# Optimization experiments

Hardware: AMD Instinct MI355X
Metric: run time of the kernel (lower is better)

Reference implementation:

```python
import jax, jax.numpy as jnp
import numpy as np
from jax import lax


def _conv1d(z, w):
    # z: [B, C_in, L], w: [C_out, C_in, K], stride 1, padding 1 -> [B, C_out, L]
    return lax.conv_general_dilated(
        z, w, window_strides=(1,), padding=[(1, 1)],
        dimension_numbers=("NCH", "OIH", "NCH"))


def setup_inputs() -> dict:
    key = jax.random.key(0)
    k1, k2, k3 = jax.random.split(key, 3)
    B, T, C, H, L, K = 16, 64, 128, 256, 128, 3
    x = jax.random.normal(k1, (B, T, C, L), dtype=jnp.float32)
    # small init so tanh stays in its useful range
    W_i = jax.random.normal(k2, (H, C, K), dtype=jnp.float32) * 0.05
    W_h = jax.random.normal(k3, (H, H, K), dtype=jnp.float32) * 0.05
    return {"x": x, "W_i": W_i, "W_h": W_h}


def reference(x, W_i, W_h):
    # Conv1DRnn, single layer, unidirectional, no bias, mode RNN_TANH:
    #   h_t = tanh(conv_i(x_t) + conv_h(h_{t-1}))
    # x: [B, T, C, L] -> out: [B, T, H, L]
    B, T, C, L = x.shape
    H = W_i.shape[0]
    h0 = jnp.zeros((B, H, L), dtype=x.dtype)
    xt = jnp.swapaxes(x, 0, 1)  # [T, B, C, L]

    def step(h, x_t):
        h_new = jnp.tanh(_conv1d(x_t, W_i) + _conv1d(h, W_h))
        return h_new, h_new

    _, hs = lax.scan(step, h0, xt)  # hs: [T, B, H, L]
    return jnp.swapaxes(hs, 0, 1)   # [B, T, H, L]
```

## Files before the change

kernel.cpp:

```cpp
#include <hip/hip_runtime.h>
#include <math.h>

typedef _Float16 f16;
typedef _Float16 f16x2 __attribute__((ext_vector_type(2)));
typedef _Float16 f16x8 __attribute__((ext_vector_type(8)));
typedef float f32x4 __attribute__((ext_vector_type(4)));
typedef unsigned long long u64;

#define LDIM 128
#define HOUT 256

#define XB0 18432

__device__ __forceinline__ float tanh_fast(float x) {
    float a = fabsf(x);
    float e = __expf(-2.0f * a);
    float r = (1.0f - e) / (1.0f + e);
    return copysignf(r, x);
}

__device__ __forceinline__ void st_mb(u64* p, u64 v) {
    __hip_atomic_store(p, v, __ATOMIC_RELAXED, __HIP_MEMORY_SCOPE_AGENT);
}
__device__ __forceinline__ u64 ld_mb(const u64* p) {
    return __hip_atomic_load(p, __ATOMIC_RELAXED, __HIP_MEMORY_SCOPE_AGENT);
}

__global__ void prep_w(const float* __restrict__ wi, f16* __restrict__ wtif,
                       const float* __restrict__ wh, f16* __restrict__ wthf)
{
    int idx = blockIdx.x * 256 + threadIdx.x;
    const int ni = 3 * 4 * 16 * 64 * 8;
    if (idx < ni) {
        int j    = idx & 7;
        int lane = (idx >> 3) & 63;
        int h16  = (idx >> 9) & 15;
        int kk   = (idx >> 13) & 3;
        int s    = idx >> 15;
        int h = h16 * 16 + (lane & 15);
        int c = kk * 32 + (lane >> 4) * 8 + j;
        wtif[idx] = (f16)wi[(h * 128 + c) * 3 + s];
    } else {
        int e = idx - ni;
        if (e >= 3 * 8 * 16 * 64 * 8) return;
        int j    = e & 7;
        int lane = (e >> 3) & 63;
        int h16  = (e >> 9) & 15;
        int kk   = (e >> 13) & 7;
        int s    = e >> 16;
        int h = h16 * 16 + (lane & 15);
        int c = kk * 32 + (lane >> 4) * 8 + j;
        wthf[e] = (f16)wh[(h * 256 + c) * 3 + s];
    }
}

__device__ __forceinline__ void stage_x(char* xp, const float* __restrict__ xt,
                                        int l0, int tid)
{
    const int c = tid >> 2, q = tid & 3;
    f32x4 v = *(const f32x4*)(xt + c * LDIM + l0 + q * 4);
#pragma unroll
    for (int i = 0; i < 4; ++i) {
        int r = q * 4 + i + 1;
        float xx = v[i];
        f16 h = (f16)xx, lo = (f16)(xx - (float)h);
        int off = r * 256 + ((((c >> 3) ^ (r & 7)) << 4)) + (c & 7) * 2;
        *(f16*)(xp + off) = h;
        *(f16*)(xp + 4608 + off) = lo;
    }
    if (tid < 256) {
        int e = tid >> 7, cc = tid & 127;
        int l = e ? l0 + 16 : l0 - 1;
        int r = e ? 17 : 0;
        float xx = ((unsigned)l < 128u) ? xt[cc * LDIM + l] : 0.f;
        f16 h = (f16)xx, lo = (f16)(xx - (float)h);
        int off = r * 256 + ((((cc >> 3) ^ (r & 7)) << 4)) + (cc & 7) * 2;
        *(f16*)(xp + off) = h;
        *(f16*)(xp + 4608 + off) = lo;
    }
}

__device__ __forceinline__ void zconv(const char* xp, const f16* __restrict__ wti,
                                      int wid, int lane, int l16, int g, f32x4 zn[2])
{
#pragma unroll
    for (int kk = 0; kk < 4; ++kk) {
#pragma unroll
        for (int s = 0; s < 3; ++s) {
            f16x8 a0 = *(const f16x8*)(wti +
                ((((s * 4 + kk) * 16 + wid * 2 + 0) * 64 + lane) << 3));
            f16x8 a1 = *(const f16x8*)(wti +
                ((((s * 4 + kk) * 16 + wid * 2 + 1) * 64 + lane) << 3));
            int r = l16 + s;
            int base = r * 256 + ((((kk * 4 + g) ^ (r & 7)) << 4));
            f16x8 b0 = *(const f16x8*)(xp + base);
            f16x8 b1 = *(const f16x8*)(xp + 4608 + base);
            zn[0] = __builtin_amdgcn_mfma_f32_16x16x32_f16(a0, b0, zn[0], 0, 0, 0);
            zn[0] = __builtin_amdgcn_mfma_f32_16x16x32_f16(a0, b1, zn[0], 0, 0, 0);
            zn[1] = __builtin_amdgcn_mfma_f32_16x16x32_f16(a1, b0, zn[1], 0, 0, 0);
            zn[1] = __builtin_amdgcn_mfma_f32_16x16x32_f16(a1, b1, zn[1], 0, 0, 0);
        }
    }
}

__device__ __forceinline__ void hconv_s(const char* hp, const f16* __restrict__ wth,
                                        int s, int wid, int lane, int l16, int g,
                                        f32x4 hacc[2])
{
#pragma unroll
    for (int kk = 0; kk < 8; ++kk) {
        f16x8 a0 = *(const f16x8*)(wth +
            ((((s * 8 + kk) * 16 + wid * 2 + 0) * 64 + lane) << 3));
        f16x8 a1 = *(const f16x8*)(wth +
            ((((s * 8 + kk) * 16 + wid * 2 + 1) * 64 + lane) << 3));
        int r = l16 + s;
        int base = r * 512 + ((((kk * 4 + g) ^ (r & 7)) << 4));
        f16x8 b0 = *(const f16x8*)(hp + base);
        hacc[0] = __builtin_amdgcn_mfma_f32_16x16x32_f16(a0, b0, hacc[0], 0, 0, 0);
        hacc[1] = __builtin_amdgcn_mfma_f32_16x16x32_f16(a1, b0, hacc[1], 0, 0, 0);
    }
}

__global__ void __launch_bounds__(512)
rnn_fused(const float* __restrict__ x, const f16* __restrict__ wti,
          const f16* __restrict__ wth, float* __restrict__ out,
          u64* __restrict__ mbox)
{
    __shared__ __align__(16) char smem[36864];
    const int tid  = threadIdx.x;
    const int lane = tid & 63, wid = tid >> 6;
    const int b    = blockIdx.x & 15;
    const int lw   = blockIdx.x >> 4;
    const int l0   = lw * 16;
    const int l16  = lane & 15, g = lane >> 4;
    const long HL  = (long)HOUT * LDIM;
    float* outb    = out + (long)b * (64 * HL);
    const float* xb = x + (long)b * (64L * 128 * LDIM);

    int edge = -1;
    if (l16 == 0  && lw > 0) edge = 0;
    if (l16 == 15 && lw < 7) edge = 1;
    u64* mb_pub = (edge >= 0) ? (mbox + (((b * 8 + lw) * 2 + edge) * 2) * 256) : nullptr;

    stage_x(smem + XB0, xb, l0, tid);
    stage_x(smem + XB0 + 9216, xb + 128 * LDIM, l0, tid);
    __syncthreads();
    f32x4 zcur[2] = {};
    zconv(smem + XB0, wti, wid, lane, l16, g, zcur);
    __syncthreads();

    for (int t = 0; t < 64; ++t) {
        float* outt = outb + (long)t * HL;

        if (t + 2 < 64)
            stage_x(smem + XB0 + (t & 1) * 9216, xb + (long)(t + 2) * (128 * LDIM), l0, tid);

        f32x4 zn[2] = {};
        if (t < 63)
            zconv(smem + XB0 + ((t + 1) & 1) * 9216, wti, wid, lane, l16, g, zn);

        f32x4 hacc[2] = {};
        char* hp = smem + ((t ^ 1) & 1) * 9216;
        if (t > 0)
            hconv_s(hp, wth, 1, wid, lane, l16, g, hacc);

        if (t > 0) {
            const int par = (t ^ 1) & 1;
            if (tid < 256) {
                int c = tid;
                float xx = 0.f;
                if (lw > 0) {
                    const u64* p = mbox + ((((b * 8 + lw - 1) * 2 + 1) * 2 + par) * 256) + c;
                    u64 v = ld_mb(p);
                    while ((unsigned)(v >> 32) < (unsigned)t) {
                        __builtin_amdgcn_s_sleep(1);
                        v = ld_mb(p);
                    }
                    xx = __uint_as_float((unsigned)v);
                }
                int off = ((c >> 3) << 4) + (c & 7) * 2;
                *(f16*)(hp + off) = (f16)xx;
            } else {
                int c = tid - 256;
                float xx = 0.f;
                if (lw < 7) {
                    const u64* p = mbox + ((((b * 8 + lw + 1) * 2 + 0) * 2 + par) * 256) + c;
                    u64 v = ld_mb(p);
                    while ((unsigned)(v >> 32) < (unsigned)t) {
                        __builtin_amdgcn_s_sleep(1);
                        v = ld_mb(p);
                    }
                    xx = __uint_as_float((unsigned)v);
                }
                int off = 17 * 512 + ((((c >> 3) ^ 1) << 4)) + (c & 7) * 2;
                *(f16*)(hp + off) = (f16)xx;
            }
        }
        __syncthreads();

        if (t > 0) {
            hconv_s(hp, wth, 0, wid, lane, l16, g, hacc);
            hconv_s(hp, wth, 2, wid, lane, l16, g, hacc);
        }

        char* pw = smem + (t & 1) * 9216;
        u64* pub = (edge >= 0) ? (mb_pub + (t & 1) * 256) : nullptr;
        const u64 tagw = ((u64)(unsigned)(t + 1)) << 32;
        const int r  = l16 + 1;
        const int rx = r & 7;
        float hv[2][4];
#pragma unroll
        for (int hf = 0; hf < 2; ++hf)
#pragma unroll
            for (int vv = 0; vv < 4; ++vv)
                hv[hf][vv] = tanh_fast(hacc[hf][vv] + zcur[hf][vv]);

        if (edge >= 0) {
#pragma unroll
            for (int hf = 0; hf < 2; ++hf)
#pragma unroll
                for (int vv = 0; vv < 4; ++vv) {
                    int c = wid * 32 + hf * 16 + g * 4 + vv;
                    st_mb(&pub[c], tagw | (u64)__float_as_uint(hv[hf][vv]));
                }
        }
#pragma unroll
        for (int hf = 0; hf < 2; ++hf)
#pragma unroll
            for (int vv = 0; vv < 4; ++vv) {
                int c = wid * 32 + hf * 16 + g * 4 + vv;
                outt[(long)c * LDIM + l0 + l16] = hv[hf][vv];
            }
#pragma unroll
        for (int hf = 0; hf < 2; ++hf)
#pragma unroll
            for (int p = 0; p < 2; ++p) {
                int c = wid * 32 + hf * 16 + g * 4 + p * 2;
                int off = r * 512 + ((((c >> 3) ^ rx) << 4)) + (c & 7) * 2;
                f16x2 hw; hw[0] = (f16)hv[hf][2 * p]; hw[1] = (f16)hv[hf][2 * p + 1];
                *(f16x2*)(pw + off) = hw;
            }
        zcur[0] = zn[0];
        zcur[1] = zn[1];

        __syncthreads();
    }
}

extern "C" void kernel_launch(void* const* d_in, const int* in_sizes, int n_in,
                              void* d_out, int out_size, void* d_ws, size_t ws_size,
                              hipStream_t stream)
{
    const float* x   = (const float*)d_in[0];
    const float* W_i = (const float*)d_in[1];
    const float* W_h = (const float*)d_in[2];
    float* out = (float*)d_out;

    f16* wt_i = (f16*)d_ws;
    f16* wt_h = (f16*)((char*)d_ws + 196608);
    u64* mbox = (u64*)((char*)d_ws + 589824);

    prep_w<<<1152, 256, 0, stream>>>(W_i, wt_i, W_h, wt_h);
    hipMemsetAsync(mbox, 0, 131072, stream);

    rnn_fused<<<128, 512, 0, stream>>>(x, wt_i, wt_h, out, mbox);
}
```

Baseline: 418.7 us.

## Use halo-widened tiles with redundant compute to exchange boundaries every 8 steps

Each block now computes a 32-column window (its 16 owned columns plus an 8-column halo on each side) so that boundary hidden states only need to be exchanged with neighbouring blocks once every 8 timesteps rather than every step. Neighbours publish 9-column packed fp16 halos through a larger mailbox, and blocks only spin-wait at those exchange points. The input-conv prefetch also drops from two steps ahead to one. The aim is to cut the per-step cross-block spin-wait latency at the cost of doubling the MFMA work per step and using more LDS and mailbox memory.

```diff
diff --git a/kernel.cpp b/kernel.cpp
--- a/kernel.cpp
+++ b/kernel.cpp
@@ -10,7 +10,7 @@
 #define LDIM 128
 #define HOUT 256
 
-#define XB0 18432
+#define XP 17408
 
 __device__ __forceinline__ float tanh_fast(float x) {
     float a = fabsf(x);
@@ -24,6 +24,10 @@
 }
 __device__ __forceinline__ u64 ld_mb(const u64* p) {
     return __hip_atomic_load(p, __ATOMIC_RELAXED, __HIP_MEMORY_SCOPE_AGENT);
+}
+__device__ __forceinline__ unsigned pack_h2(float a, float b) {
+    f16x2 t; t[0] = (f16)a; t[1] = (f16)b;
+    unsigned u; __builtin_memcpy(&u, &t, 4); return u;
 }
 
 __global__ void prep_w(const float* __restrict__ wi, f16* __restrict__ wtif,
@@ -58,66 +62,30 @@
                                         int l0, int tid)
 {
     const int c = tid >> 2, q = tid & 3;
-    f32x4 v = *(const f32x4*)(xt + c * LDIM + l0 + q * 4);
-#pragma unroll
-    for (int i = 0; i < 4; ++i) {
-        int r = q * 4 + i + 1;
-        float xx = v[i];
+    const int colStart = l0 - 8 + q * 8;
+    f32x4 v0 = {}, v1 = {};
+    if (colStart >= 0 && colStart + 7 < 128) {
+        v0 = *(const f32x4*)(xt + c * LDIM + colStart);
+        v1 = *(const f32x4*)(xt + c * LDIM + colStart + 4);
+    }
+#pragma unroll
+    for (int i = 0; i < 8; ++i) {
+        int row = q * 8 + i + 1;
+        float xx = (i < 4) ? v0[i] : v1[i - 4];
         f16 h = (f16)xx, lo = (f16)(xx - (float)h);
-        int off = r * 256 + ((((c >> 3) ^ (r & 7)) << 4)) + (c & 7) * 2;
+        int off = row * 256 + ((((c >> 3) ^ (row & 7)) << 4)) + (c & 7) * 2;
         *(f16*)(xp + off) = h;
-        *(f16*)(xp + 4608 + off) = lo;
+        *(f16*)(xp + 8704 + off) = lo;
     }
     if (tid < 256) {
-        int e = tid >> 7, cc = tid & 127;
-        int l = e ? l0 + 16 : l0 - 1;
-        int r = e ? 17 : 0;
-        float xx = ((unsigned)l < 128u) ? xt[cc * LDIM + l] : 0.f;
+        int row = (tid >= 128) ? 33 : 0;
+        int cc  = tid & 127;
+        int col = (row == 0) ? l0 - 9 : l0 + 24;
+        float xx = ((unsigned)col < 128u) ? xt[cc * LDIM + col] : 0.f;
         f16 h = (f16)xx, lo = (f16)(xx - (float)h);
-        int off = r * 256 + ((((cc >> 3) ^ (r & 7)) << 4)) + (cc & 7) * 2;
+        int off = row * 256 + ((((cc >> 3) ^ (row & 7)) << 4)) + (cc & 7) * 2;
         *(f16*)(xp + off) = h;
-        *(f16*)(xp + 4608 + off) = lo;
-    }
-}
-
-__device__ __forceinline__ void zconv(const char* xp, const f16* __restrict__ wti,
-                                      int wid, int lane, int l16, int g, f32x4 zn[2])
-{
-#pragma unroll
-    for (int kk = 0; kk < 4; ++kk) {
-#pragma unroll
-        for (int s = 0; s < 3; ++s) {
-            f16x8 a0 = *(const f16x8*)(wti +
-                ((((s * 4 + kk) * 16 + wid * 2 + 0) * 64 + lane) << 3));
-            f16x8 a1 = *(const f16x8*)(wti +
-                ((((s * 4 + kk) * 16 + wid * 2 + 1) * 64 + lane) << 3));
-            int r = l16 + s;
-            int base = r * 256 + ((((kk * 4 + g) ^ (r & 7)) << 4));
-            f16x8 b0 = *(const f16x8*)(xp + base);
-            f16x8 b1 = *(const f16x8*)(xp + 4608 + base);
-            zn[0] = __builtin_amdgcn_mfma_f32_16x16x32_f16(a0, b0, zn[0], 0, 0, 0);
-            zn[0] = __builtin_amdgcn_mfma_f32_16x16x32_f16(a0, b1, zn[0], 0, 0, 0);
-            zn[1] = __builtin_amdgcn_mfma_f32_16x16x32_f16(a1, b0, zn[1], 0, 0, 0);
-            zn[1] = __builtin_amdgcn_mfma_f32_16x16x32_f16(a1, b1, zn[1], 0, 0, 0);
-        }
-    }
-}
-
-__device__ __forceinline__ void hconv_s(const char* hp, const f16* __restrict__ wth,
-                                        int s, int wid, int lane, int l16, int g,
-                                        f32x4 hacc[2])
-{
-#pragma unroll
-    for (int kk = 0; kk < 8; ++kk) {
-        f16x8 a0 = *(const f16x8*)(wth +
-            ((((s * 8 + kk) * 16 + wid * 2 + 0) * 64 + lane) << 3));
-        f16x8 a1 = *(const f16x8*)(wth +
-            ((((s * 8 + kk) * 16 + wid * 2 + 1) * 64 + lane) << 3));
-        int r = l16 + s;
-        int base = r * 512 + ((((kk * 4 + g) ^ (r & 7)) << 4));
-        f16x8 b0 = *(const f16x8*)(hp + base);
-        hacc[0] = __builtin_amdgcn_mfma_f32_16x16x32_f16(a0, b0, hacc[0], 0, 0, 0);
-        hacc[1] = __builtin_amdgcn_mfma_f32_16x16x32_f16(a1, b0, hacc[1], 0, 0, 0);
+        *(f16*)(xp + 8704 + off) = lo;
     }
 }
 
@@ -126,7 +94,7 @@
           const f16* __restrict__ wth, float* __restrict__ out,
           u64* __restrict__ mbox)
 {
-    __shared__ __align__(16) char smem[36864];
+    __shared__ __align__(16) char smem[52224];
     const int tid  = threadIdx.x;
     const int lane = tid & 63, wid = tid >> 6;
     const int b    = blockIdx.x & 15;
@@ -137,113 +105,168 @@
     float* outb    = out + (long)b * (64 * HL);
     const float* xb = x + (long)b * (64L * 128 * LDIM);
 
-    int edge = -1;
-    if (l16 == 0  && lw > 0) edge = 0;
-    if (l16 == 15 && lw < 7) edge = 1;
-    u64* mb_pub = (edge >= 0) ? (mbox + (((b * 8 + lw) * 2 + edge) * 2) * 256) : nullptr;
-
-    stage_x(smem + XB0, xb, l0, tid);
-    stage_x(smem + XB0 + 9216, xb + 128 * LDIM, l0, tid);
-    __syncthreads();
-    f32x4 zcur[2] = {};
-    zconv(smem + XB0, wti, wid, lane, l16, g, zcur);
+    {
+        int row = (tid >= 256) ? 33 : 0;
+        int cc  = tid & 255;
+        int off = row * 512 + ((((cc >> 3) ^ (row & 7)) << 4)) + (cc & 7) * 2;
+        *(f16*)(smem + off) = (f16)0.f;
+    }
+    stage_x(smem + XP, xb, l0, tid);
     __syncthreads();
 
     for (int t = 0; t < 64; ++t) {
         float* outt = outb + (long)t * HL;
 
-        if (t + 2 < 64)
-            stage_x(smem + XB0 + (t & 1) * 9216, xb + (long)(t + 2) * (128 * LDIM), l0, tid);
-
-        f32x4 zn[2] = {};
-        if (t < 63)
-            zconv(smem + XB0 + ((t + 1) & 1) * 9216, wti, wid, lane, l16, g, zn);
-
-        f32x4 hacc[2] = {};
-        char* hp = smem + ((t ^ 1) & 1) * 9216;
-        if (t > 0)
-            hconv_s(hp, wth, 1, wid, lane, l16, g, hacc);
-
+        if (t + 1 < 64)
+            stage_x(smem + XP + ((t + 1) & 1) * 17408,
+                    xb + (long)(t + 1) * (128 * LDIM), l0, tid);
+
+        f32x4 zcur[2][2] = {};
+        {
+            const char* xp = smem + XP + (t & 1) * 17408;
+#pragma unroll
+            for (int kk = 0; kk < 4; ++kk)
+#pragma unroll
+                for (int s = 0; s < 3; ++s) {
+                    f16x8 a0 = *(const f16x8*)(wti +
+                        ((((s * 4 + kk) * 16 + wid * 2 + 0) * 64 + lane) << 3));
+                    f16x8 a1 = *(const f16x8*)(wti +
+                        ((((s * 4 + kk) * 16 + wid * 2 + 1) * 64 + lane) << 3));
+#pragma unroll
+                    for (int tau = 0; tau < 2; ++tau) {
+                        int r = 16 * tau + l16 + s;
+                        int base = r * 256 + ((((kk * 4 + g) ^ (r & 7)) << 4));
+                        f16x8 bh = *(const f16x8*)(xp + base);
+                        f16x8 bl = *(const f16x8*)(xp + 8704 + base);
+                        zcur[tau][0] = __builtin_amdgcn_mfma_f32_16x16x32_f16(a0, bh, zcur[tau][0], 0, 0, 0);
+                        zcur[tau][0] = __builtin_amdgcn_mfma_f32_16x16x32_f16(a0, bl, zcur[tau][0], 0, 0, 0);
+                        zcur[tau][1] = __builtin_amdgcn_mfma_f32_16x16x32_f16(a1, bh, zcur[tau][1], 0, 0, 0);
+                        zcur[tau][1] = __builtin_amdgcn_mfma_f32_16x16x32_f16(a1, bl, zcur[tau][1], 0, 0, 0);
+                    }
+                }
+        }
+
+        f32x4 hacc[2][2] = {};
         if (t > 0) {
-            const int par = (t ^ 1) & 1;
-            if (tid < 256) {
-                int c = tid;
-                float xx = 0.f;
-                if (lw > 0) {
-                    const u64* p = mbox + ((((b * 8 + lw - 1) * 2 + 1) * 2 + par) * 256) + c;
+#pragma unroll
+            for (int kk = 0; kk < 8; ++kk)
+#pragma unroll
+                for (int s = 0; s < 3; ++s) {
+                    f16x8 a0 = *(const f16x8*)(wth +
+                        ((((s * 8 + kk) * 16 + wid * 2 + 0) * 64 + lane) << 3));
+                    f16x8 a1 = *(const f16x8*)(wth +
+                        ((((s * 8 + kk) * 16 + wid * 2 + 1) * 64 + lane) << 3));
+#pragma unroll
+                    for (int tau = 0; tau < 2; ++tau) {
+                        int r = 16 * tau + l16 + s;
+                        int base = r * 512 + ((((kk * 4 + g) ^ (r & 7)) << 4));
+                        f16x8 bb = *(const f16x8*)(smem + base);
+                        hacc[tau][0] = __builtin_amdgcn_mfma_f32_16x16x32_f16(a0, bb, hacc[tau][0], 0, 0, 0);
+                        hacc[tau][1] = __builtin_amdgcn_mfma_f32_16x16x32_f16(a1, bb, hacc[tau][1], 0, 0, 0);
+                    }
+                }
+        }
+        __syncthreads();
+
+        float hv[2][2][4];
+#pragma unroll
+        for (int tau = 0; tau < 2; ++tau)
+#pragma unroll
+            for (int hf = 0; hf < 2; ++hf)
+#pragma unroll
+                for (int vv = 0; vv < 4; ++vv)
+                    hv[tau][hf][vv] = tanh_fast(hacc[tau][hf][vv] + zcur[tau][hf][vv]);
+
+        {
+            const int tsel = (l16 < 8) ? 1 : 0;
+            const int gcs  = l0 + (l16 ^ 8);
+#pragma unroll
+            for (int hf = 0; hf < 2; ++hf)
+#pragma unroll
+                for (int vv = 0; vv < 4; ++vv) {
+                    int c = wid * 32 + hf * 16 + g * 4 + vv;
+                    outt[(long)c * LDIM + gcs] = hv[tsel][hf][vv];
+                }
+        }
+#pragma unroll
+        for (int tau = 0; tau < 2; ++tau) {
+            const int rw = 1 + 16 * tau + l16;
+            const int gc = l0 - 9 + rw;
+            const bool ok = ((unsigned)gc < 128u);
+            const int rx = rw & 7;
+#pragma unroll
+            for (int hf = 0; hf < 2; ++hf)
+#pragma unroll
+                for (int p = 0; p < 2; ++p) {
+                    int c = wid * 32 + hf * 16 + g * 4 + p * 2;
+                    f16x2 w;
+                    w[0] = ok ? (f16)hv[tau][hf][2 * p]     : (f16)0.f;
+                    w[1] = ok ? (f16)hv[tau][hf][2 * p + 1] : (f16)0.f;
+                    int off = rw * 512 + ((((c >> 3) ^ rx) << 4)) + (c & 7) * 2;
+                    *(f16x2*)(smem + off) = w;
+                }
+        }
+        __syncthreads();
+
+        if (t > 0 && (t & 7) == 0 && t <= 56) {
+            const unsigned e = (unsigned)(t >> 3);
+            const int par = e & 1;
+            const u64 tagw = ((u64)e) << 32;
+
+            {
+                int cs = -1, tl = 0;
+                if (l16 >= 8)      { cs = l16 - 8; tl = 0; }
+                else if (l16 == 0) { cs = 8;       tl = 1; }
+                if (cs >= 0 && lw > 0) {
+                    u64* mp = mbox + (((long)(b * 8 + lw) * 2 + 0) * 2 + par) * 1152 + cs * 128;
+#pragma unroll
+                    for (int hf = 0; hf < 2; ++hf)
+#pragma unroll
+                        for (int p = 0; p < 2; ++p) {
+                            int hp = wid * 16 + hf * 8 + g * 2 + p;
+                            st_mb(mp + hp, tagw |
+                                  (u64)pack_h2(hv[tl][hf][2 * p], hv[tl][hf][2 * p + 1]));
+                        }
+                }
+            }
+            {
+                int cs = -1, tr_ = 0;
+                if (l16 == 15)     { cs = 0;        tr_ = 0; }
+                else if (l16 <= 7) { cs = l16 + 1;  tr_ = 1; }
+                if (cs >= 0 && lw < 7) {
+                    u64* mp = mbox + (((long)(b * 8 + lw) * 2 + 1) * 2 + par) * 1152 + cs * 128;
+#pragma unroll
+                    for (int hf = 0; hf < 2; ++hf)
+#pragma unroll
+                        for (int p = 0; p < 2; ++p) {
+                            int hp = wid * 16 + hf * 8 + g * 2 + p;
+                            st_mb(mp + hp, tagw |
+                                  (u64)pack_h2(hv[tr_][hf][2 * p], hv[tr_][hf][2 * p + 1]));
+                        }
+                }
+            }
+            for (int i = tid; i < 2304; i += 512) {
+                int side = (i >= 1152);
+                int j = i - side * 1152;
+                int col = j >> 7, hp = j & 127;
+                int nb = lw + (side ? 1 : -1);
+                if ((unsigned)nb < 8u) {
+                    const u64* p = mbox + (((long)(b * 8 + nb) * 2 + (side ? 0 : 1)) * 2 + par) * 1152 + j;
                     u64 v = ld_mb(p);
-                    while ((unsigned)(v >> 32) < (unsigned)t) {
+                    while ((unsigned)(v >> 32) < e) {
                         __builtin_amdgcn_s_sleep(1);
                         v = ld_mb(p);
                     }
-                    xx = __uint_as_float((unsigned)v);
-                }
-                int off = ((c >> 3) << 4) + (c & 7) * 2;
-                *(f16*)(hp + off) = (f16)xx;
-            } else {
-                int c = tid - 256;
-                float xx = 0.f;
-                if (lw < 7) {
-                    const u64* p = mbox + ((((b * 8 + lw + 1) * 2 + 0) * 2 + par) * 256) + c;
-                    u64 v = ld_mb(p);
-                    while ((unsigned)(v >> 32) < (unsigned)t) {
-                        __builtin_amdgcn_s_sleep(1);
-                        v = ld_mb(p);
-                    }
-                    xx = __uint_as_float((unsigned)v);
-                }
-                int off = 17 * 512 + ((((c >> 3) ^ 1) << 4)) + (c & 7) * 2;
-                *(f16*)(hp + off) = (f16)xx;
+                    unsigned pk = (unsigned)v;
+                    int row = side ? 25 + col : col;
+                    int c = hp * 2;
+                    int off = row * 512 + ((((c >> 3) ^ (row & 7)) << 4)) + (c & 7) * 2;
+                    f16x2 w; __builtin_memcpy(&w, &pk, 4);
+                    *(f16x2*)(smem + off) = w;
+                }
             }
-        }
-        __syncthreads();
-
-        if (t > 0) {
-            hconv_s(hp, wth, 0, wid, lane, l16, g, hacc);
-            hconv_s(hp, wth, 2, wid, lane, l16, g, hacc);
-        }
-
-        char* pw = smem + (t & 1) * 9216;
-        u64* pub = (edge >= 0) ? (mb_pub + (t & 1) * 256) : nullptr;
-        const u64 tagw = ((u64)(unsigned)(t + 1)) << 32;
-        const int r  = l16 + 1;
-        const int rx = r & 7;
-        float hv[2][4];
-#pragma unroll
-        for (int hf = 0; hf < 2; ++hf)
-#pragma unroll
-            for (int vv = 0; vv < 4; ++vv)
-                hv[hf][vv] = tanh_fast(hacc[hf][vv] + zcur[hf][vv]);
-
-        if (edge >= 0) {
-#pragma unroll
-            for (int hf = 0; hf < 2; ++hf)
-#pragma unroll
-                for (int vv = 0; vv < 4; ++vv) {
-                    int c = wid * 32 + hf * 16 + g * 4 + vv;
-                    st_mb(&pub[c], tagw | (u64)__float_as_uint(hv[hf][vv]));
-                }
-        }
-#pragma unroll
-        for (int hf = 0; hf < 2; ++hf)
-#pragma unroll
-            for (int vv = 0; vv < 4; ++vv) {
-                int c = wid * 32 + hf * 16 + g * 4 + vv;
-                outt[(long)c * LDIM + l0 + l16] = hv[hf][vv];
-            }
-#pragma unroll
-        for (int hf = 0; hf < 2; ++hf)
-#pragma unroll
-            for (int p = 0; p < 2; ++p) {
-                int c = wid * 32 + hf * 16 + g * 4 + p * 2;
-                int off = r * 512 + ((((c >> 3) ^ rx) << 4)) + (c & 7) * 2;
-                f16x2 hw; hw[0] = (f16)hv[hf][2 * p]; hw[1] = (f16)hv[hf][2 * p + 1];
-                *(f16x2*)(pw + off) = hw;
-            }
-        zcur[0] = zn[0];
-        zcur[1] = zn[1];
-
-        __syncthreads();
+            __syncthreads();
+        }
     }
 }
 
@@ -261,7 +284,7 @@
     u64* mbox = (u64*)((char*)d_ws + 589824);
 
     prep_w<<<1152, 256, 0, stream>>>(W_i, wt_i, W_h, wt_h);
-    hipMemsetAsync(mbox, 0, 131072, stream);
+    hipMemsetAsync(mbox, 0, 4718592, stream);
 
     rnn_fused<<<128, 512, 0, stream>>>(x, wt_i, wt_h, out, mbox);
 }
```

Result: slower. 572.9 us (+36.8%).

## Keep recurrent weights in registers with 4 waves and drop x split-precision

Applied to the files above, without the earlier changes.

Cuts the block to 256 threads (4 waves, each covering 64 output channels) and preloads all W_h MFMA fragments into registers once, so the per-step recurrent conv no longer reloads weights from global memory. The x-input conv is computed inline each step into the same accumulator instead of being pipelined a step ahead. The hi/lo fp16 split of x is dropped, which halves the MFMA work for the input conv but lowers input precision. The register footprint is very large (96 f16x8 fragments per lane), which risks spills, and there are half as many waves to hide latency.

```diff
diff --git a/kernel.cpp b/kernel.cpp
--- a/kernel.cpp
+++ b/kernel.cpp
@@ -10,7 +10,7 @@
 #define LDIM 128
 #define HOUT 256
 
-#define XB0 18432
+#define XB 18432
 
 __device__ __forceinline__ float tanh_fast(float x) {
     float a = fabsf(x);
@@ -57,76 +57,23 @@
 __device__ __forceinline__ void stage_x(char* xp, const float* __restrict__ xt,
                                         int l0, int tid)
 {
-    const int c = tid >> 2, q = tid & 3;
-    f32x4 v = *(const f32x4*)(xt + c * LDIM + l0 + q * 4);
-#pragma unroll
-    for (int i = 0; i < 4; ++i) {
-        int r = q * 4 + i + 1;
-        float xx = v[i];
-        f16 h = (f16)xx, lo = (f16)(xx - (float)h);
-        int off = r * 256 + ((((c >> 3) ^ (r & 7)) << 4)) + (c & 7) * 2;
-        *(f16*)(xp + off) = h;
-        *(f16*)(xp + 4608 + off) = lo;
+    const int c = tid & 127, half = tid >> 7;
+#pragma unroll
+    for (int i = 0; i < 9; ++i) {
+        int row = half * 9 + i;
+        int col = l0 - 1 + row;
+        float xx = ((unsigned)col < 128u) ? xt[c * LDIM + col] : 0.f;
+        int off = row * 256 + ((((c >> 3) ^ (row & 7)) << 4)) + (c & 7) * 2;
+        *(f16*)(xp + off) = (f16)xx;
     }
-    if (tid < 256) {
-        int e = tid >> 7, cc = tid & 127;
-        int l = e ? l0 + 16 : l0 - 1;
-        int r = e ? 17 : 0;
-        float xx = ((unsigned)l < 128u) ? xt[cc * LDIM + l] : 0.f;
-        f16 h = (f16)xx, lo = (f16)(xx - (float)h);
-        int off = r * 256 + ((((cc >> 3) ^ (r & 7)) << 4)) + (cc & 7) * 2;
-        *(f16*)(xp + off) = h;
-        *(f16*)(xp + 4608 + off) = lo;
-    }
-}
-
-__device__ __forceinline__ void zconv(const char* xp, const f16* __restrict__ wti,
-                                      int wid, int lane, int l16, int g, f32x4 zn[2])
-{
-#pragma unroll
-    for (int kk = 0; kk < 4; ++kk) {
-#pragma unroll
-        for (int s = 0; s < 3; ++s) {
-            f16x8 a0 = *(const f16x8*)(wti +
-                ((((s * 4 + kk) * 16 + wid * 2 + 0) * 64 + lane) << 3));
-            f16x8 a1 = *(const f16x8*)(wti +
-                ((((s * 4 + kk) * 16 + wid * 2 + 1) * 64 + lane) << 3));
-            int r = l16 + s;
-            int base = r * 256 + ((((kk * 4 + g) ^ (r & 7)) << 4));
-            f16x8 b0 = *(const f16x8*)(xp + base);
-            f16x8 b1 = *(const f16x8*)(xp + 4608 + base);
-            zn[0] = __builtin_amdgcn_mfma_f32_16x16x32_f16(a0, b0, zn[0], 0, 0, 0);
-            zn[0] = __builtin_amdgcn_mfma_f32_16x16x32_f16(a0, b1, zn[0], 0, 0, 0);
-            zn[1] = __builtin_amdgcn_mfma_f32_16x16x32_f16(a1, b0, zn[1], 0, 0, 0);
-            zn[1] = __builtin_amdgcn_mfma_f32_16x16x32_f16(a1, b1, zn[1], 0, 0, 0);
-        }
-    }
-}
-
-__device__ __forceinline__ void hconv_s(const char* hp, const f16* __restrict__ wth,
-                                        int s, int wid, int lane, int l16, int g,
-                                        f32x4 hacc[2])
-{
-#pragma unroll
-    for (int kk = 0; kk < 8; ++kk) {
-        f16x8 a0 = *(const f16x8*)(wth +
-            ((((s * 8 + kk) * 16 + wid * 2 + 0) * 64 + lane) << 3));
-        f16x8 a1 = *(const f16x8*)(wth +
-            ((((s * 8 + kk) * 16 + wid * 2 + 1) * 64 + lane) << 3));
-        int r = l16 + s;
-        int base = r * 512 + ((((kk * 4 + g) ^ (r & 7)) << 4));
-        f16x8 b0 = *(const f16x8*)(hp + base);
-        hacc[0] = __builtin_amdgcn_mfma_f32_16x16x32_f16(a0, b0, hacc[0], 0, 0, 0);
-        hacc[1] = __builtin_amdgcn_mfma_f32_16x16x32_f16(a1, b0, hacc[1], 0, 0, 0);
-    }
-}
-
-__global__ void __launch_bounds__(512)
+}
+
+__global__ void __launch_bounds__(256, 1)
 rnn_fused(const float* __restrict__ x, const f16* __restrict__ wti,
           const f16* __restrict__ wth, float* __restrict__ out,
           u64* __restrict__ mbox)
 {
-    __shared__ __align__(16) char smem[36864];
+    __shared__ __align__(16) char smem[27648];
     const int tid  = threadIdx.x;
     const int lane = tid & 63, wid = tid >> 6;
     const int b    = blockIdx.x & 15;
@@ -142,35 +89,76 @@
     if (l16 == 15 && lw < 7) edge = 1;
     u64* mb_pub = (edge >= 0) ? (mbox + (((b * 8 + lw) * 2 + edge) * 2) * 256) : nullptr;
 
-    stage_x(smem + XB0, xb, l0, tid);
-    stage_x(smem + XB0 + 9216, xb + 128 * LDIM, l0, tid);
-    __syncthreads();
-    f32x4 zcur[2] = {};
-    zconv(smem + XB0, wti, wid, lane, l16, g, zcur);
+    f16x8 afrh[3][8][4];
+#pragma unroll
+    for (int s = 0; s < 3; ++s)
+#pragma unroll
+        for (int kk = 0; kk < 8; ++kk)
+#pragma unroll
+            for (int hf = 0; hf < 4; ++hf)
+                afrh[s][kk][hf] = *(const f16x8*)(wth +
+                    ((((s * 8 + kk) * 16 + wid * 4 + hf) * 64 + lane) << 3));
+
+    stage_x(smem + XB, xb, l0, tid);
     __syncthreads();
 
     for (int t = 0; t < 64; ++t) {
         float* outt = outb + (long)t * HL;
 
-        if (t + 2 < 64)
-            stage_x(smem + XB0 + (t & 1) * 9216, xb + (long)(t + 2) * (128 * LDIM), l0, tid);
-
-        f32x4 zn[2] = {};
-        if (t < 63)
-            zconv(smem + XB0 + ((t + 1) & 1) * 9216, wti, wid, lane, l16, g, zn);
-
-        f32x4 hacc[2] = {};
+        if (t + 1 < 64)
+            stage_x(smem + XB + ((t + 1) & 1) * 4608,
+                    xb + (long)(t + 1) * (128 * LDIM), l0, tid);
+
+        f32x4 acc[4] = {};
+        {
+            const char* xp = smem + XB + (t & 1) * 4608;
+#pragma unroll
+            for (int kk = 0; kk < 4; ++kk)
+#pragma unroll
+                for (int s = 0; s < 3; ++s) {
+                    f16x8 a0 = *(const f16x8*)(wti +
+                        ((((s * 4 + kk) * 16 + wid * 4 + 0) * 64 + lane) << 3));
+                    f16x8 a1 = *(const f16x8*)(wti +
+                        ((((s * 4 + kk) * 16 + wid * 4 + 1) * 64 + lane) << 3));
+                    f16x8 a2 = *(const f16x8*)(wti +
+                        ((((s * 4 + kk) * 16 + wid * 4 + 2) * 64 + lane) << 3));
+                    f16x8 a3 = *(const f16x8*)(wti +
+                        ((((s * 4 + kk) * 16 + wid * 4 + 3) * 64 + lane) << 3));
+                    int r = l16 + s;
+                    int base = r * 256 + ((((kk * 4 + g) ^ (r & 7)) << 4));
+                    f16x8 bb = *(const f16x8*)(xp + base);
+                    acc[0] = __builtin_amdgcn_mfma_f32_16x16x32_f16(a0, bb, acc[0], 0, 0, 0);
+                    acc[1] = __builtin_amdgcn_mfma_f32_16x16x32_f16(a1, bb, acc[1], 0, 0, 0);
+                    acc[2] = __builtin_amdgcn_mfma_f32_16x16x32_f16(a2, bb, acc[2], 0, 0, 0);
+                    acc[3] = __builtin_amdgcn_mfma_f32_16x16x32_f16(a3, bb, acc[3], 0, 0, 0);
+                }
+        }
+
         char* hp = smem + ((t ^ 1) & 1) * 9216;
-        if (t > 0)
-            hconv_s(hp, wth, 1, wid, lane, l16, g, hacc);
+
+        if (t > 0) {
+#pragma unroll
+            for (int kk = 0; kk < 8; ++kk) {
+                int r = l16 + 1;
+                int base = r * 512 + ((((kk * 4 + g) ^ (r & 7)) << 4));
+                f16x8 bb = *(const f16x8*)(hp + base);
+#pragma unroll
+                for (int hf = 0; hf < 4; ++hf)
+                    acc[hf] = __builtin_amdgcn_mfma_f32_16x16x32_f16(
+                        afrh[1][kk][hf], bb, acc[hf], 0, 0, 0);
+            }
+        }
 
         if (t > 0) {
             const int par = (t ^ 1) & 1;
-            if (tid < 256) {
+#pragma unroll
+            for (int side = 0; side < 2; ++side) {
                 int c = tid;
+                int nb = lw + (side ? 1 : -1);
                 float xx = 0.f;
-                if (lw > 0) {
-                    const u64* p = mbox + ((((b * 8 + lw - 1) * 2 + 1) * 2 + par) * 256) + c;
+                if ((unsigned)nb < 8u) {
+                    const u64* p = mbox +
+                        ((((b * 8 + nb) * 2 + (side ? 0 : 1)) * 2 + par) * 256) + c;
                     u64 v = ld_mb(p);
                     while ((unsigned)(v >> 32) < (unsigned)t) {
                         __builtin_amdgcn_s_sleep(1);
@@ -178,70 +166,66 @@
                     }
                     xx = __uint_as_float((unsigned)v);
                 }
-                int off = ((c >> 3) << 4) + (c & 7) * 2;
+                int row = side ? 17 : 0;
+                int off = row * 512 + ((((c >> 3) ^ (row & 7)) << 4)) + (c & 7) * 2;
                 *(f16*)(hp + off) = (f16)xx;
-            } else {
-                int c = tid - 256;
-                float xx = 0.f;
-                if (lw < 7) {
-                    const u64* p = mbox + ((((b * 8 + lw + 1) * 2 + 0) * 2 + par) * 256) + c;
-                    u64 v = ld_mb(p);
-                    while ((unsigned)(v >> 32) < (unsigned)t) {
-                        __builtin_amdgcn_s_sleep(1);
-                        v = ld_mb(p);
-                    }
-                    xx = __uint_as_float((unsigned)v);
-                }
-                int off = 17 * 512 + ((((c >> 3) ^ 1) << 4)) + (c & 7) * 2;
-                *(f16*)(hp + off) = (f16)xx;
             }
         }
         __syncthreads();
 
         if (t > 0) {
-            hconv_s(hp, wth, 0, wid, lane, l16, g, hacc);
-            hconv_s(hp, wth, 2, wid, lane, l16, g, hacc);
+#pragma unroll
+            for (int kk = 0; kk < 8; ++kk)
+#pragma unroll
+                for (int sp = 0; sp < 2; ++sp) {
+                    int s = sp * 2;
+                    int r = l16 + s;
+                    int base = r * 512 + ((((kk * 4 + g) ^ (r & 7)) << 4));
+                    f16x8 bb = *(const f16x8*)(hp + base);
+#pragma unroll
+                    for (int hf = 0; hf < 4; ++hf)
+                        acc[hf] = __builtin_amdgcn_mfma_f32_16x16x32_f16(
+                            afrh[s][kk][hf], bb, acc[hf], 0, 0, 0);
+                }
         }
 
         char* pw = smem + (t & 1) * 9216;
         u64* pub = (edge >= 0) ? (mb_pub + (t & 1) * 256) : nullptr;
         const u64 tagw = ((u64)(unsigned)(t + 1)) << 32;
-        const int r  = l16 + 1;
-        const int rx = r & 7;
-        float hv[2][4];
-#pragma unroll
-        for (int hf = 0; hf < 2; ++hf)
+        const int rw = l16 + 1;
+        const int rx = rw & 7;
+        float hv[4][4];
+#pragma unroll
+        for (int hf = 0; hf < 4; ++hf)
 #pragma unroll
             for (int vv = 0; vv < 4; ++vv)
-                hv[hf][vv] = tanh_fast(hacc[hf][vv] + zcur[hf][vv]);
+                hv[hf][vv] = tanh_fast(acc[hf][vv]);
 
         if (edge >= 0) {
 #pragma unroll
-            for (int hf = 0; hf < 2; ++hf)
+            for (int hf = 0; hf < 4; ++hf)
 #pragma unroll
                 for (int vv = 0; vv < 4; ++vv) {
-                    int c = wid * 32 + hf * 16 + g * 4 + vv;
+                    int c = wid * 64 + hf * 16 + g * 4 + vv;
                     st_mb(&pub[c], tagw | (u64)__float_as_uint(hv[hf][vv]));
                 }
         }
 #pragma unroll
-        for (int hf = 0; hf < 2; ++hf)
+        for (int hf = 0; hf < 4; ++hf)
 #pragma unroll
             for (int vv = 0; vv < 4; ++vv) {
-                int c = wid * 32 + hf * 16 + g * 4 + vv;
+                int c = wid * 64 + hf * 16 + g * 4 + vv;
                 outt[(long)c * LDIM + l0 + l16] = hv[hf][vv];
             }
 #pragma unroll
-        for (int hf = 0; hf < 2; ++hf)
+        for (int hf = 0; hf < 4; ++hf)
 #pragma unroll
             for (int p = 0; p < 2; ++p) {
-                int c = wid * 32 + hf * 16 + g * 4 + p * 2;
-                int off = r * 512 + ((((c >> 3) ^ rx) << 4)) + (c & 7) * 2;
+                int c = wid * 64 + hf * 16 + g * 4 + p * 2;
+                int off = rw * 512 + ((((c >> 3) ^ rx) << 4)) + (c & 7) * 2;
                 f16x2 hw; hw[0] = (f16)hv[hf][2 * p]; hw[1] = (f16)hv[hf][2 * p + 1];
                 *(f16x2*)(pw + off) = hw;
             }
-        zcur[0] = zn[0];
-        zcur[1] = zn[1];
 
         __syncthreads();
     }
@@ -263,5 +247,5 @@
     prep_w<<<1152, 256, 0, stream>>>(W_i, wt_i, W_h, wt_h);
     hipMemsetAsync(mbox, 0, 131072, stream);
 
-    rnn_fused<<<128, 512, 0, stream>>>(x, wt_i, wt_h, out, mbox);
-}
+    rnn_fused<<<128, 256, 0, stream>>>(x, wt_i, wt_h, out, mbox);
+}
```

Result: slower. 1.511 ms (+260.8%).
